# Kernel optimization log

Hardware: AMD Instinct MI355X
Metric: run time of the kernel (lower is better)

## Reference

```python
import jax, jax.numpy as jnp
import numpy as np

BIG = 1e20  # sentinel used by the original code for out-of-window positions


def setup_inputs() -> dict:
    key = jax.random.key(0)
    k1, k2, k3 = jax.random.split(key, 3)
    B, C, L, K = 8, 256, 4096, 8
    x = jax.random.normal(k1, (B, C, L), dtype=jnp.float32)
    delta_time = jax.random.uniform(k2, (B, L), dtype=jnp.float32)
    kernel_total = jax.random.uniform(k3, (1, 1, K), dtype=jnp.float32)  # nn.Parameter torch.rand
    return {"x": x, "delta_time": delta_time, "kernel_total": kernel_total}


def reference(x, delta_time, kernel_total):
    # x: (B, C, L); delta_time: (B, L); kernel_total: (1, 1, K)
    K = kernel_total.shape[-1]
    L = x.shape[-1]
    pos = jnp.arange(L)

    # Causal sliding window: shift i rolls right by i; first i positions masked.
    rolled_x = jnp.stack(
        [jnp.where(pos < i, 0.0, jnp.roll(x, i, axis=2)) for i in range(K)], axis=-1
    )  # (B, C, L, K)
    dts = jnp.stack(
        [jnp.where(pos < i, BIG, jnp.roll(delta_time, i, axis=1)) - delta_time
         for i in range(K)], axis=-1
    )  # (B, L, K)

    w_time = jax.nn.softmax(dts, axis=-1)[:, None]          # (B, 1, L, K)
    average_time = (rolled_x * w_time).sum(axis=-1)          # (B, C, L)
    average_previous = (rolled_x * kernel_total).sum(axis=-1)  # (B, C, L)

    average = jnp.stack([average_time, average_previous], axis=-2)  # (B, C, 2, L)
    scores = jax.nn.softmax(
        jnp.einsum("bcil,bcjl->bcij", average, average), axis=-1
    )  # (B, C, 2, 2)
    out = jnp.einsum("bcij,bcjl->bcil", scores, average).mean(axis=-2)  # (B, C, L)
    return out
```

## Files before the change

### kernel.cpp

```cpp
#include <hip/hip_runtime.h>

#define BIG 1e20f

__global__ __launch_bounds__(256) void wtime_kernel(const float* __restrict__ dt,
                                                    float* __restrict__ w,
                                                    int B, int L) {
    int idx = blockIdx.x * 256 + threadIdx.x;
    int b = idx >> 12;
    int l = idx & (L - 1);
    const float* dtb = dt + (size_t)b * L;
    float dtl = dtb[l];

    float v[8];
#pragma unroll
    for (int k = 0; k < 8; ++k) {
        v[k] = (l < k) ? (BIG - dtl) : (dtb[l - k] - dtl);
    }
    float m = v[0];
#pragma unroll
    for (int k = 1; k < 8; ++k) m = fmaxf(m, v[k]);
    float s = 0.f;
#pragma unroll
    for (int k = 0; k < 8; ++k) { v[k] = __expf(v[k] - m); s += v[k]; }
    float inv = 1.f / s;

#pragma unroll
    for (int k = 0; k < 8; ++k)
        w[((size_t)b * 8 + k) * L + l] = v[k] * inv;
}

__global__ __launch_bounds__(256) void main_kernel(const float* __restrict__ x,
                                                   const float* __restrict__ w,
                                                   const float* __restrict__ ker,
                                                   float* __restrict__ out,
                                                   int C, int L) {
    const int pair = blockIdx.x;
    const int b    = pair >> 7;
    const int c0   = (pair & 127) << 1;
    const int tid  = threadIdx.x;

    const float* x0 = x + ((size_t)b * C + c0) * L;
    const float* x1 = x0 + L;
    const float* wb = w + (size_t)b * 8 * L;
    float*       o0 = out + ((size_t)b * C + c0) * L;
    float*       o1 = o0 + L;

    float kk[8];
#pragma unroll
    for (int k = 0; k < 8; ++k) kk[k] = ker[k];

    float tv0[16], pv0[16], tv1[16], pv1[16];
    float gtt0 = 0.f, gtp0 = 0.f, gpp0 = 0.f;
    float gtt1 = 0.f, gtp1 = 0.f, gpp1 = 0.f;

#pragma unroll
    for (int g = 0; g < 4; ++g) {
        const int l0 = g * 1024 + tid * 4;

        float xr0[12], xr1[12];
        if (g == 0 && tid < 2) {
            if (tid == 0) {
#pragma unroll
                for (int i = 0; i < 8; ++i) { xr0[i] = 0.f; xr1[i] = 0.f; }
            } else {
#pragma unroll
                for (int i = 0; i < 4; ++i) { xr0[i] = 0.f; xr1[i] = 0.f; }
                float4 a = *reinterpret_cast<const float4*>(x0 + 0);
                float4 b4 = *reinterpret_cast<const float4*>(x1 + 0);
                xr0[4] = a.x;  xr0[5] = a.y;  xr0[6] = a.z;  xr0[7] = a.w;
                xr1[4] = b4.x; xr1[5] = b4.y; xr1[6] = b4.z; xr1[7] = b4.w;
            }
        } else {
            float4 a0 = *reinterpret_cast<const float4*>(x0 + l0 - 8);
            float4 c4 = *reinterpret_cast<const float4*>(x0 + l0 - 4);
            xr0[0] = a0.x; xr0[1] = a0.y; xr0[2] = a0.z; xr0[3] = a0.w;
            xr0[4] = c4.x; xr0[5] = c4.y; xr0[6] = c4.z; xr0[7] = c4.w;
            float4 a1 = *reinterpret_cast<const float4*>(x1 + l0 - 8);
            float4 c1 = *reinterpret_cast<const float4*>(x1 + l0 - 4);
            xr1[0] = a1.x; xr1[1] = a1.y; xr1[2] = a1.z; xr1[3] = a1.w;
            xr1[4] = c1.x; xr1[5] = c1.y; xr1[6] = c1.z; xr1[7] = c1.w;
        }
        {
            float4 d0 = *reinterpret_cast<const float4*>(x0 + l0);
            xr0[8] = d0.x; xr0[9] = d0.y; xr0[10] = d0.z; xr0[11] = d0.w;
            float4 d1 = *reinterpret_cast<const float4*>(x1 + l0);
            xr1[8] = d1.x; xr1[9] = d1.y; xr1[10] = d1.z; xr1[11] = d1.w;
        }

        float t0[4] = {0.f, 0.f, 0.f, 0.f}, p0[4] = {0.f, 0.f, 0.f, 0.f};
        float t1[4] = {0.f, 0.f, 0.f, 0.f}, p1[4] = {0.f, 0.f, 0.f, 0.f};
#pragma unroll
        for (int k = 0; k < 8; ++k) {
            float4 wv = *reinterpret_cast<const float4*>(wb + (size_t)k * L + l0);
            float wk4[4] = {wv.x, wv.y, wv.z, wv.w};
#pragma unroll
            for (int j = 0; j < 4; ++j) {
                float xv0 = xr0[8 + j - k];
                float xv1 = xr1[8 + j - k];
                t0[j] = fmaf(xv0, wk4[j], t0[j]);
                p0[j] = fmaf(xv0, kk[k], p0[j]);
                t1[j] = fmaf(xv1, wk4[j], t1[j]);
                p1[j] = fmaf(xv1, kk[k], p1[j]);
            }
        }
#pragma unroll
        for (int j = 0; j < 4; ++j) {
            tv0[g * 4 + j] = t0[j];  pv0[g * 4 + j] = p0[j];
            tv1[g * 4 + j] = t1[j];  pv1[g * 4 + j] = p1[j];
            gtt0 = fmaf(t0[j], t0[j], gtt0);
            gtp0 = fmaf(t0[j], p0[j], gtp0);
            gpp0 = fmaf(p0[j], p0[j], gpp0);
            gtt1 = fmaf(t1[j], t1[j], gtt1);
            gtp1 = fmaf(t1[j], p1[j], gtp1);
            gpp1 = fmaf(p1[j], p1[j], gpp1);
        }
    }

    float gr[6] = {gtt0, gtp0, gpp0, gtt1, gtp1, gpp1};
#pragma unroll
    for (int off = 32; off > 0; off >>= 1) {
#pragma unroll
        for (int i = 0; i < 6; ++i) gr[i] += __shfl_down(gr[i], off);
    }
    __shared__ float red[6][4];
    const int wave = tid >> 6;
    if ((tid & 63) == 0) {
#pragma unroll
        for (int i = 0; i < 6; ++i) red[i][wave] = gr[i];
    }
    __syncthreads();
    float G[6];
#pragma unroll
    for (int i = 0; i < 6; ++i) G[i] = red[i][0] + red[i][1] + red[i][2] + red[i][3];

    float ct[2], cp[2];
#pragma unroll
    for (int ch = 0; ch < 2; ++ch) {
        const float Gtt = G[ch * 3 + 0], Gtp = G[ch * 3 + 1], Gpp = G[ch * 3 + 2];
        const float m0 = fmaxf(Gtt, Gtp);
        const float e00 = __expf(Gtt - m0), e01 = __expf(Gtp - m0);
        const float r0 = 1.f / (e00 + e01);
        const float m1 = fmaxf(Gtp, Gpp);
        const float e10 = __expf(Gtp - m1), e11 = __expf(Gpp - m1);
        const float r1 = 1.f / (e10 + e11);
        ct[ch] = 0.5f * (e00 * r0 + e10 * r1);
        cp[ch] = 0.5f * (e01 * r0 + e11 * r1);
    }

#pragma unroll
    for (int g = 0; g < 4; ++g) {
        const int l0 = g * 1024 + tid * 4;
        float4 oa, ob;
        oa.x = fmaf(ct[0], tv0[g * 4 + 0], cp[0] * pv0[g * 4 + 0]);
        oa.y = fmaf(ct[0], tv0[g * 4 + 1], cp[0] * pv0[g * 4 + 1]);
        oa.z = fmaf(ct[0], tv0[g * 4 + 2], cp[0] * pv0[g * 4 + 2]);
        oa.w = fmaf(ct[0], tv0[g * 4 + 3], cp[0] * pv0[g * 4 + 3]);
        *reinterpret_cast<float4*>(o0 + l0) = oa;
        ob.x = fmaf(ct[1], tv1[g * 4 + 0], cp[1] * pv1[g * 4 + 0]);
        ob.y = fmaf(ct[1], tv1[g * 4 + 1], cp[1] * pv1[g * 4 + 1]);
        ob.z = fmaf(ct[1], tv1[g * 4 + 2], cp[1] * pv1[g * 4 + 2]);
        ob.w = fmaf(ct[1], tv1[g * 4 + 3], cp[1] * pv1[g * 4 + 3]);
        *reinterpret_cast<float4*>(o1 + l0) = ob;
    }
}

extern "C" void kernel_launch(void* const* d_in, const int* in_sizes, int n_in,
                              void* d_out, int out_size, void* d_ws, size_t ws_size,
                              hipStream_t stream) {
    const float* x   = (const float*)d_in[0];
    const float* dt  = (const float*)d_in[1];
    const float* ker = (const float*)d_in[2];
    float* out = (float*)d_out;

    const int B = 8, C = 256, L = 4096;
    float* w = (float*)d_ws;

    wtime_kernel<<<(B * L) / 256, 256, 0, stream>>>(dt, w, B, L);
    main_kernel<<<(B * C) / 2, 256, 0, stream>>>(x, w, ker, out, C, L);
}
```

Baseline: 96.03 us.

## Fuse time-weight softmax into main kernel and use 512-thread blocks

Drops the separate kernel that wrote the 8xL softmax weights to workspace. The main kernel now loads delta_time directly and recomputes the softmax weights per position. Blocks grow to 512 threads, each handling 2 groups of 4 positions instead of 4. This saves one launch and the write and reread of the weight buffer, at the cost of repeating the exp and softmax work for every channel pair, 128 times per batch.

```diff
diff --git a/kernel.cpp b/kernel.cpp
--- a/kernel.cpp
+++ b/kernel.cpp
@@ -2,73 +2,47 @@
 
 #define BIG 1e20f
 
-__global__ __launch_bounds__(256) void wtime_kernel(const float* __restrict__ dt,
-                                                    float* __restrict__ w,
-                                                    int B, int L) {
-    int idx = blockIdx.x * 256 + threadIdx.x;
-    int b = idx >> 12;
-    int l = idx & (L - 1);
-    const float* dtb = dt + (size_t)b * L;
-    float dtl = dtb[l];
-
-    float v[8];
-#pragma unroll
-    for (int k = 0; k < 8; ++k) {
-        v[k] = (l < k) ? (BIG - dtl) : (dtb[l - k] - dtl);
-    }
-    float m = v[0];
-#pragma unroll
-    for (int k = 1; k < 8; ++k) m = fmaxf(m, v[k]);
-    float s = 0.f;
-#pragma unroll
-    for (int k = 0; k < 8; ++k) { v[k] = __expf(v[k] - m); s += v[k]; }
-    float inv = 1.f / s;
-
-#pragma unroll
-    for (int k = 0; k < 8; ++k)
-        w[((size_t)b * 8 + k) * L + l] = v[k] * inv;
-}
-
-__global__ __launch_bounds__(256) void main_kernel(const float* __restrict__ x,
-                                                   const float* __restrict__ w,
-                                                   const float* __restrict__ ker,
-                                                   float* __restrict__ out,
-                                                   int C, int L) {
+__global__ __launch_bounds__(512) void fused_kernel(const float* __restrict__ x,
+                                                    const float* __restrict__ dt,
+                                                    const float* __restrict__ ker,
+                                                    float* __restrict__ out,
+                                                    int C, int L) {
     const int pair = blockIdx.x;
     const int b    = pair >> 7;
     const int c0   = (pair & 127) << 1;
     const int tid  = threadIdx.x;
 
-    const float* x0 = x + ((size_t)b * C + c0) * L;
-    const float* x1 = x0 + L;
-    const float* wb = w + (size_t)b * 8 * L;
-    float*       o0 = out + ((size_t)b * C + c0) * L;
-    float*       o1 = o0 + L;
+    const float* x0  = x + ((size_t)b * C + c0) * L;
+    const float* x1  = x0 + L;
+    const float* dtb = dt + (size_t)b * L;
+    float*       o0  = out + ((size_t)b * C + c0) * L;
+    float*       o1  = o0 + L;
 
     float kk[8];
 #pragma unroll
     for (int k = 0; k < 8; ++k) kk[k] = ker[k];
 
-    float tv0[16], pv0[16], tv1[16], pv1[16];
-    float gtt0 = 0.f, gtp0 = 0.f, gpp0 = 0.f;
-    float gtt1 = 0.f, gtp1 = 0.f, gpp1 = 0.f;
+    float tv0[8], pv0[8], tv1[8], pv1[8];
+    float gr[6] = {0.f, 0.f, 0.f, 0.f, 0.f, 0.f};
 
 #pragma unroll
-    for (int g = 0; g < 4; ++g) {
-        const int l0 = g * 1024 + tid * 4;
+    for (int g = 0; g < 2; ++g) {
+        const int l0 = g * 2048 + tid * 4;
 
-        float xr0[12], xr1[12];
+        float xr0[12], xr1[12], dtr[12];
         if (g == 0 && tid < 2) {
             if (tid == 0) {
 #pragma unroll
-                for (int i = 0; i < 8; ++i) { xr0[i] = 0.f; xr1[i] = 0.f; }
+                for (int i = 0; i < 8; ++i) { xr0[i] = 0.f; xr1[i] = 0.f; dtr[i] = BIG; }
             } else {
 #pragma unroll
-                for (int i = 0; i < 4; ++i) { xr0[i] = 0.f; xr1[i] = 0.f; }
+                for (int i = 0; i < 4; ++i) { xr0[i] = 0.f; xr1[i] = 0.f; dtr[i] = BIG; }
                 float4 a = *reinterpret_cast<const float4*>(x0 + 0);
-                float4 b4 = *reinterpret_cast<const float4*>(x1 + 0);
+                float4 bb = *reinterpret_cast<const float4*>(x1 + 0);
+                float4 d = *reinterpret_cast<const float4*>(dtb + 0);
                 xr0[4] = a.x;  xr0[5] = a.y;  xr0[6] = a.z;  xr0[7] = a.w;
-                xr1[4] = b4.x; xr1[5] = b4.y; xr1[6] = b4.z; xr1[7] = b4.w;
+                xr1[4] = bb.x; xr1[5] = bb.y; xr1[6] = bb.z; xr1[7] = bb.w;
+                dtr[4] = d.x;  dtr[5] = d.y;  dtr[6] = d.z;  dtr[7] = d.w;
             }
         } else {
             float4 a0 = *reinterpret_cast<const float4*>(x0 + l0 - 8);
@@ -79,50 +53,62 @@
             float4 c1 = *reinterpret_cast<const float4*>(x1 + l0 - 4);
             xr1[0] = a1.x; xr1[1] = a1.y; xr1[2] = a1.z; xr1[3] = a1.w;
             xr1[4] = c1.x; xr1[5] = c1.y; xr1[6] = c1.z; xr1[7] = c1.w;
+            float4 d0 = *reinterpret_cast<const float4*>(dtb + l0 - 8);
+            float4 d1 = *reinterpret_cast<const float4*>(dtb + l0 - 4);
+            dtr[0] = d0.x; dtr[1] = d0.y; dtr[2] = d0.z; dtr[3] = d0.w;
+            dtr[4] = d1.x; dtr[5] = d1.y; dtr[6] = d1.z; dtr[7] = d1.w;
         }
         {
-            float4 d0 = *reinterpret_cast<const float4*>(x0 + l0);
-            xr0[8] = d0.x; xr0[9] = d0.y; xr0[10] = d0.z; xr0[11] = d0.w;
-            float4 d1 = *reinterpret_cast<const float4*>(x1 + l0);
-            xr1[8] = d1.x; xr1[9] = d1.y; xr1[10] = d1.z; xr1[11] = d1.w;
+            float4 e0 = *reinterpret_cast<const float4*>(x0 + l0);
+            xr0[8] = e0.x; xr0[9] = e0.y; xr0[10] = e0.z; xr0[11] = e0.w;
+            float4 e1 = *reinterpret_cast<const float4*>(x1 + l0);
+            xr1[8] = e1.x; xr1[9] = e1.y; xr1[10] = e1.z; xr1[11] = e1.w;
+            float4 ed = *reinterpret_cast<const float4*>(dtb + l0);
+            dtr[8] = ed.x; dtr[9] = ed.y; dtr[10] = ed.z; dtr[11] = ed.w;
         }
 
-        float t0[4] = {0.f, 0.f, 0.f, 0.f}, p0[4] = {0.f, 0.f, 0.f, 0.f};
-        float t1[4] = {0.f, 0.f, 0.f, 0.f}, p1[4] = {0.f, 0.f, 0.f, 0.f};
-#pragma unroll
-        for (int k = 0; k < 8; ++k) {
-            float4 wv = *reinterpret_cast<const float4*>(wb + (size_t)k * L + l0);
-            float wk4[4] = {wv.x, wv.y, wv.z, wv.w};
-#pragma unroll
-            for (int j = 0; j < 4; ++j) {
-                float xv0 = xr0[8 + j - k];
-                float xv1 = xr1[8 + j - k];
-                t0[j] = fmaf(xv0, wk4[j], t0[j]);
-                p0[j] = fmaf(xv0, kk[k], p0[j]);
-                t1[j] = fmaf(xv1, wk4[j], t1[j]);
-                p1[j] = fmaf(xv1, kk[k], p1[j]);
-            }
-        }
 #pragma unroll
         for (int j = 0; j < 4; ++j) {
-            tv0[g * 4 + j] = t0[j];  pv0[g * 4 + j] = p0[j];
-            tv1[g * 4 + j] = t1[j];  pv1[g * 4 + j] = p1[j];
-            gtt0 = fmaf(t0[j], t0[j], gtt0);
-            gtp0 = fmaf(t0[j], p0[j], gtp0);
-            gpp0 = fmaf(p0[j], p0[j], gpp0);
-            gtt1 = fmaf(t1[j], t1[j], gtt1);
-            gtp1 = fmaf(t1[j], p1[j], gtp1);
-            gpp1 = fmaf(p1[j], p1[j], gpp1);
+            const float dtl = dtr[8 + j];
+            float v[8];
+#pragma unroll
+            for (int k = 0; k < 8; ++k) v[k] = dtr[8 + j - k] - dtl;
+            float m = v[0];
+#pragma unroll
+            for (int k = 1; k < 8; ++k) m = fmaxf(m, v[k]);
+            float s = 0.f;
+#pragma unroll
+            for (int k = 0; k < 8; ++k) { v[k] = __expf(v[k] - m); s += v[k]; }
+            const float inv = 1.f / s;
+
+            float t0 = 0.f, p0 = 0.f, t1 = 0.f, p1 = 0.f;
+#pragma unroll
+            for (int k = 0; k < 8; ++k) {
+                const float wk  = v[k] * inv;
+                const float xa  = xr0[8 + j - k];
+                const float xb  = xr1[8 + j - k];
+                t0 = fmaf(xa, wk, t0);
+                p0 = fmaf(xa, kk[k], p0);
+                t1 = fmaf(xb, wk, t1);
+                p1 = fmaf(xb, kk[k], p1);
+            }
+            tv0[g * 4 + j] = t0;  pv0[g * 4 + j] = p0;
+            tv1[g * 4 + j] = t1;  pv1[g * 4 + j] = p1;
+            gr[0] = fmaf(t0, t0, gr[0]);
+            gr[1] = fmaf(t0, p0, gr[1]);
+            gr[2] = fmaf(p0, p0, gr[2]);
+            gr[3] = fmaf(t1, t1, gr[3]);
+            gr[4] = fmaf(t1, p1, gr[4]);
+            gr[5] = fmaf(p1, p1, gr[5]);
         }
     }
 
-    float gr[6] = {gtt0, gtp0, gpp0, gtt1, gtp1, gpp1};
 #pragma unroll
     for (int off = 32; off > 0; off >>= 1) {
 #pragma unroll
         for (int i = 0; i < 6; ++i) gr[i] += __shfl_down(gr[i], off);
     }
-    __shared__ float red[6][4];
+    __shared__ float red[6][8];
     const int wave = tid >> 6;
     if ((tid & 63) == 0) {
 #pragma unroll
@@ -131,7 +117,12 @@
     __syncthreads();
     float G[6];
 #pragma unroll
-    for (int i = 0; i < 6; ++i) G[i] = red[i][0] + red[i][1] + red[i][2] + red[i][3];
+    for (int i = 0; i < 6; ++i) {
+        float acc = 0.f;
+#pragma unroll
+        for (int wv = 0; wv < 8; ++wv) acc += red[i][wv];
+        G[i] = acc;
+    }
 
     float ct[2], cp[2];
 #pragma unroll
@@ -148,8 +139,8 @@
     }
 
 #pragma unroll
-    for (int g = 0; g < 4; ++g) {
-        const int l0 = g * 1024 + tid * 4;
+    for (int g = 0; g < 2; ++g) {
+        const int l0 = g * 2048 + tid * 4;
         float4 oa, ob;
         oa.x = fmaf(ct[0], tv0[g * 4 + 0], cp[0] * pv0[g * 4 + 0]);
         oa.y = fmaf(ct[0], tv0[g * 4 + 1], cp[0] * pv0[g * 4 + 1]);
@@ -173,8 +164,5 @@
     float* out = (float*)d_out;
 
     const int B = 8, C = 256, L = 4096;
-    float* w = (float*)d_ws;
-
-    wtime_kernel<<<(B * L) / 256, 256, 0, stream>>>(dt, w, B, L);
-    main_kernel<<<(B * C) / 2, 256, 0, stream>>>(x, w, ker, out, C, L);
+    fused_kernel<<<(B * C) / 2, 512, 0, stream>>>(x, dt, ker, out, C, L);
 }
```

Result: no change. 94.52 us (-1.6%).
